# Kernel optimization log

Measured on AMD Instinct MI355X. Metric: run time of the kernel, lower is better.

## Reference

```python
import jax, jax.numpy as jnp
import numpy as np

GROUP = 128  # quantization group size along the input dimension


def dequant(q, scales, zeros):
    # q: [out, in] int4 codes stored as int32 in [0,16)
    # scales, zeros: [out, in//GROUP] per-group affine params
    out_dim, in_dim = q.shape
    g = in_dim // GROUP
    w = (q.astype(jnp.float32).reshape(out_dim, g, GROUP) - zeros[:, :, None]) * scales[:, :, None]
    return w.reshape(out_dim, in_dim)


def setup_inputs() -> dict:
    key = jax.random.key(0)
    ks = jax.random.split(key, 10)
    H, I = 4096, 11008
    B, S = 64, 1
    inp = {
        "x": jax.random.normal(ks[0], (B, S, H), dtype=jnp.float32),
        "gate_qweight": jax.random.randint(ks[1], (I, H), 0, 16, dtype=jnp.int32),
        "gate_scales": jax.random.uniform(ks[2], (I, H // GROUP), dtype=jnp.float32) * 0.02,
        "gate_zeros": jax.random.uniform(ks[3], (I, H // GROUP), dtype=jnp.float32) * 16.0,
        "up_qweight": jax.random.randint(ks[4], (I, H), 0, 16, dtype=jnp.int32),
        "up_scales": jax.random.uniform(ks[5], (I, H // GROUP), dtype=jnp.float32) * 0.02,
        "up_zeros": jax.random.uniform(ks[6], (I, H // GROUP), dtype=jnp.float32) * 16.0,
        "down_qweight": jax.random.randint(ks[7], (H, I), 0, 16, dtype=jnp.int32),
        "down_scales": jax.random.uniform(ks[8], (H, I // GROUP), dtype=jnp.float32) * 0.02,
        "down_zeros": jax.random.uniform(ks[9], (H, I // GROUP), dtype=jnp.float32) * 16.0,
    }
    return inp


def reference(x, gate_qweight, gate_scales, gate_zeros,
              up_qweight, up_scales, up_zeros,
              down_qweight, down_scales, down_zeros):
    Wg = dequant(gate_qweight, gate_scales, gate_zeros)   # [I, H]
    Wu = dequant(up_qweight, up_scales, up_zeros)         # [I, H]
    Wd = dequant(down_qweight, down_scales, down_zeros)   # [H, I]
    gate = jnp.einsum('bsh,ih->bsi', x, Wg)
    up = jnp.einsum('bsh,ih->bsi', x, Wu)
    h = jax.nn.silu(gate) * up                             # SwiGLU
    return jnp.einsum('bsi,hi->bsh', h, Wd)
```

## Files before the change

kernel.cpp:

```cpp
#include <hip/hip_runtime.h>
#include <stdint.h>

#define H_DIM 4096
#define I_DIM 11008
#define NGH   (H_DIM/128)
#define NGI   (I_DIM/128)

typedef __attribute__((ext_vector_type(8))) short short8;
typedef __attribute__((ext_vector_type(4))) float f32x4;
typedef __attribute__((ext_vector_type(4))) int   i32x4;

static __device__ __forceinline__ short f2bf(float f) {
  uint32_t u = __builtin_bit_cast(uint32_t, f);
  u = (u + 0x7FFFu + ((u >> 16) & 1u)) >> 16;
  return (short)(uint16_t)u;
}

__global__ void xcvt_kernel(const float* __restrict__ x, short* __restrict__ xb) {
  int i = blockIdx.x * 256 + threadIdx.x;
  xb[i] = f2bf(x[i]);
}

__global__ __launch_bounds__(256) void phase1_kernel(
    const short* __restrict__ xb,
    const int* __restrict__ gq, const float* __restrict__ gsc, const float* __restrict__ gze,
    const int* __restrict__ uq, const float* __restrict__ usc, const float* __restrict__ uze,
    short* __restrict__ hb)
{
  __shared__ float red[2][4][4][4][64];
  const int n0   = blockIdx.x * 16;
  const int w    = threadIdx.x >> 6;
  const int l    = threadIdx.x & 63;
  const int col  = l & 15;
  const int krow = l >> 4;
  const int i    = n0 + col;

  const int*   gqr = gq + (size_t)i * H_DIM;
  const int*   uqr = uq + (size_t)i * H_DIM;
  const float* gsr = gsc + (size_t)i * NGH;
  const float* gzr = gze + (size_t)i * NGH;
  const float* usr = usc + (size_t)i * NGH;
  const float* uzr = uze + (size_t)i * NGH;

  f32x4 accG[4], accU[4];
#pragma unroll
  for (int c = 0; c < 4; ++c)
#pragma unroll
    for (int r = 0; r < 4; ++r) { accG[c][r] = 0.f; accU[c][r] = 0.f; }

  const int g0 = w * 8;
#pragma unroll 1
  for (int g = g0; g < g0 + 8; ++g) {
    const float sg = gsr[g], zg = gzr[g] * sg;
    const float su = usr[g], zu = uzr[g] * su;
#pragma unroll
    for (int ks = 0; ks < 4; ++ks) {
      const int koff = g * 128 + ks * 32 + krow * 8;
      short8 a[4];
#pragma unroll
      for (int c = 0; c < 4; ++c)
        a[c] = *(const short8*)(xb + (size_t)(c * 16 + col) * H_DIM + koff);
      i32x4 q0 = *(const i32x4*)(gqr + koff);
      i32x4 q1 = *(const i32x4*)(gqr + koff + 4);
      i32x4 p0 = *(const i32x4*)(uqr + koff);
      i32x4 p1 = *(const i32x4*)(uqr + koff + 4);
      short8 bg, bu;
#pragma unroll
      for (int j = 0; j < 4; ++j) {
        bg[j]     = f2bf((float)q0[j] * sg - zg);
        bg[j + 4] = f2bf((float)q1[j] * sg - zg);
        bu[j]     = f2bf((float)p0[j] * su - zu);
        bu[j + 4] = f2bf((float)p1[j] * su - zu);
      }
#pragma unroll
      for (int c = 0; c < 4; ++c) {
        accG[c] = __builtin_amdgcn_mfma_f32_16x16x32_bf16(a[c], bg, accG[c], 0, 0, 0);
        accU[c] = __builtin_amdgcn_mfma_f32_16x16x32_bf16(a[c], bu, accU[c], 0, 0, 0);
      }
    }
  }

#pragma unroll
  for (int c = 0; c < 4; ++c)
#pragma unroll
    for (int r = 0; r < 4; ++r) {
      red[0][w][c][r][l] = accG[c][r];
      red[1][w][c][r][l] = accU[c][r];
    }
  __syncthreads();

  {
    const int c  = threadIdx.x >> 6;
    const int ll = threadIdx.x & 63;
#pragma unroll
    for (int r = 0; r < 4; ++r) {
      float gsum = red[0][0][c][r][ll] + red[0][1][c][r][ll]
                 + red[0][2][c][r][ll] + red[0][3][c][r][ll];
      float usum = red[1][0][c][r][ll] + red[1][1][c][r][ll]
                 + red[1][2][c][r][ll] + red[1][3][c][r][ll];
      float hv = gsum / (1.f + __expf(-gsum)) * usum;
      const int m  = c * 16 + (ll >> 4) * 4 + r;
      const int ii = n0 + (ll & 15);
      hb[(size_t)m * I_DIM + ii] = f2bf(hv);
    }
  }
}

__global__ __launch_bounds__(512) void phase2_kernel(
    const short* __restrict__ hb,
    const int* __restrict__ dq, const float* __restrict__ dsc, const float* __restrict__ dze,
    float* __restrict__ out)
{
  __shared__ float red[8][4][4][64];
  const int n0   = blockIdx.x * 16;
  const int w    = threadIdx.x >> 6;
  const int l    = threadIdx.x & 63;
  const int col  = l & 15;
  const int krow = l >> 4;
  const int n    = n0 + col;

  const int*   dqr = dq + (size_t)n * I_DIM;
  const float* dsr = dsc + (size_t)n * NGI;
  const float* dzr = dze + (size_t)n * NGI;

  f32x4 acc[4];
#pragma unroll
  for (int c = 0; c < 4; ++c)
#pragma unroll
    for (int r = 0; r < 4; ++r) acc[c][r] = 0.f;

  const int kbeg = w * (I_DIM / 8);
  int gprev = -1;
  float sv = 0.f, zv = 0.f;
#pragma unroll 1
  for (int ks = 0; ks < 43; ++ks) {
    const int k0 = kbeg + ks * 32;
    const int g  = k0 >> 7;
    if (g != gprev) { sv = dsr[g]; zv = dzr[g] * sv; gprev = g; }
    const int koff = k0 + krow * 8;
    short8 a[4];
#pragma unroll
    for (int c = 0; c < 4; ++c)
      a[c] = *(const short8*)(hb + (size_t)(c * 16 + col) * I_DIM + koff);
    i32x4 q0 = *(const i32x4*)(dqr + koff);
    i32x4 q1 = *(const i32x4*)(dqr + koff + 4);
    short8 b;
#pragma unroll
    for (int j = 0; j < 4; ++j) {
      b[j]     = f2bf((float)q0[j] * sv - zv);
      b[j + 4] = f2bf((float)q1[j] * sv - zv);
    }
#pragma unroll
    for (int c = 0; c < 4; ++c)
      acc[c] = __builtin_amdgcn_mfma_f32_16x16x32_bf16(a[c], b, acc[c], 0, 0, 0);
  }

#pragma unroll
  for (int c = 0; c < 4; ++c)
#pragma unroll
    for (int r = 0; r < 4; ++r)
      red[w][c][r][l] = acc[c][r];
  __syncthreads();

  if (threadIdx.x < 256) {
    const int c  = threadIdx.x >> 6;
    const int ll = threadIdx.x & 63;
#pragma unroll
    for (int r = 0; r < 4; ++r) {
      float s = 0.f;
#pragma unroll
      for (int ww = 0; ww < 8; ++ww) s += red[ww][c][r][ll];
      const int m  = c * 16 + (ll >> 4) * 4 + r;
      const int nn = n0 + (ll & 15);
      out[(size_t)m * H_DIM + nn] = s;
    }
  }
}

extern "C" void kernel_launch(void* const* d_in, const int* in_sizes, int n_in,
                              void* d_out, int out_size, void* d_ws, size_t ws_size,
                              hipStream_t stream) {
  const float* x  = (const float*)d_in[0];
  const int*   gq = (const int*)d_in[1];
  const float* gs = (const float*)d_in[2];
  const float* gz = (const float*)d_in[3];
  const int*   uq = (const int*)d_in[4];
  const float* us = (const float*)d_in[5];
  const float* uz = (const float*)d_in[6];
  const int*   dq = (const int*)d_in[7];
  const float* ds = (const float*)d_in[8];
  const float* dz = (const float*)d_in[9];
  float* out = (float*)d_out;

  short* xb = (short*)d_ws;
  short* hb = (short*)((char*)d_ws + (size_t)64 * H_DIM * 2);

  xcvt_kernel<<<(64 * H_DIM) / 256, 256, 0, stream>>>(x, xb);
  phase1_kernel<<<I_DIM / 16, 256, 0, stream>>>(xb, gq, gs, gz, uq, us, uz, hb);
  phase2_kernel<<<H_DIM / 16, 512, 0, stream>>>(hb, dq, ds, dz, out);
}
```

Before: 208.9 us.

## Split-K down projection, 8-wave gate/up blocks, weight prefetch, vectorized convert

Phase 2 now runs a four-way split over the intermediate dimension, launching four times as many blocks, and adds a reduce kernel that sums the partial outputs. Phase 1 moves to 512-thread blocks with eight waves splitting K and reduces gate and up through shared memory in two passes. Both phases software-prefetch the next quantized weight chunk into registers, and the x conversion is vectorized four-wide using the HIP bf16 intrinsic. The goal is more parallelism to saturate HBM on the weight stream. The cost is extra partial-buffer traffic and one more launch.

```diff
diff --git a/kernel.cpp b/kernel.cpp
--- a/kernel.cpp
+++ b/kernel.cpp
@@ -1,4 +1,5 @@
 #include <hip/hip_runtime.h>
+#include <hip/hip_bf16.h>
 #include <stdint.h>
 
 #define H_DIM 4096
@@ -7,109 +8,29 @@
 #define NGI   (I_DIM/128)
 
 typedef __attribute__((ext_vector_type(8))) short short8;
+typedef __attribute__((ext_vector_type(4))) short s16x4;
 typedef __attribute__((ext_vector_type(4))) float f32x4;
 typedef __attribute__((ext_vector_type(4))) int   i32x4;
 
 static __device__ __forceinline__ short f2bf(float f) {
-  uint32_t u = __builtin_bit_cast(uint32_t, f);
-  u = (u + 0x7FFFu + ((u >> 16) & 1u)) >> 16;
-  return (short)(uint16_t)u;
+  union { __hip_bfloat16 b; short s; } u;
+  u.b = __float2bfloat16(f);
+  return u.s;
 }
 
 __global__ void xcvt_kernel(const float* __restrict__ x, short* __restrict__ xb) {
-  int i = blockIdx.x * 256 + threadIdx.x;
-  xb[i] = f2bf(x[i]);
-}
-
-__global__ __launch_bounds__(256) void phase1_kernel(
+  int i = (blockIdx.x * 256 + threadIdx.x) * 4;
+  f32x4 v = *(const f32x4*)(x + i);
+  s16x4 o;
+  o[0] = f2bf(v[0]); o[1] = f2bf(v[1]); o[2] = f2bf(v[2]); o[3] = f2bf(v[3]);
+  *(s16x4*)(xb + i) = o;
+}
+
+__global__ __launch_bounds__(512, 4) void phase1_kernel(
     const short* __restrict__ xb,
     const int* __restrict__ gq, const float* __restrict__ gsc, const float* __restrict__ gze,
     const int* __restrict__ uq, const float* __restrict__ usc, const float* __restrict__ uze,
     short* __restrict__ hb)
-{
-  __shared__ float red[2][4][4][4][64];
-  const int n0   = blockIdx.x * 16;
-  const int w    = threadIdx.x >> 6;
-  const int l    = threadIdx.x & 63;
-  const int col  = l & 15;
-  const int krow = l >> 4;
-  const int i    = n0 + col;
-
-  const int*   gqr = gq + (size_t)i * H_DIM;
-  const int*   uqr = uq + (size_t)i * H_DIM;
-  const float* gsr = gsc + (size_t)i * NGH;
-  const float* gzr = gze + (size_t)i * NGH;
-  const float* usr = usc + (size_t)i * NGH;
-  const float* uzr = uze + (size_t)i * NGH;
-
-  f32x4 accG[4], accU[4];
-#pragma unroll
-  for (int c = 0; c < 4; ++c)
-#pragma unroll
-    for (int r = 0; r < 4; ++r) { accG[c][r] = 0.f; accU[c][r] = 0.f; }
-
-  const int g0 = w * 8;
-#pragma unroll 1
-  for (int g = g0; g < g0 + 8; ++g) {
-    const float sg = gsr[g], zg = gzr[g] * sg;
-    const float su = usr[g], zu = uzr[g] * su;
-#pragma unroll
-    for (int ks = 0; ks < 4; ++ks) {
-      const int koff = g * 128 + ks * 32 + krow * 8;
-      short8 a[4];
-#pragma unroll
-      for (int c = 0; c < 4; ++c)
-        a[c] = *(const short8*)(xb + (size_t)(c * 16 + col) * H_DIM + koff);
-      i32x4 q0 = *(const i32x4*)(gqr + koff);
-      i32x4 q1 = *(const i32x4*)(gqr + koff + 4);
-      i32x4 p0 = *(const i32x4*)(uqr + koff);
-      i32x4 p1 = *(const i32x4*)(uqr + koff + 4);
-      short8 bg, bu;
-#pragma unroll
-      for (int j = 0; j < 4; ++j) {
-        bg[j]     = f2bf((float)q0[j] * sg - zg);
-        bg[j + 4] = f2bf((float)q1[j] * sg - zg);
-        bu[j]     = f2bf((float)p0[j] * su - zu);
-        bu[j + 4] = f2bf((float)p1[j] * su - zu);
-      }
-#pragma unroll
-      for (int c = 0; c < 4; ++c) {
-        accG[c] = __builtin_amdgcn_mfma_f32_16x16x32_bf16(a[c], bg, accG[c], 0, 0, 0);
-        accU[c] = __builtin_amdgcn_mfma_f32_16x16x32_bf16(a[c], bu, accU[c], 0, 0, 0);
-      }
-    }
-  }
-
-#pragma unroll
-  for (int c = 0; c < 4; ++c)
-#pragma unroll
-    for (int r = 0; r < 4; ++r) {
-      red[0][w][c][r][l] = accG[c][r];
-      red[1][w][c][r][l] = accU[c][r];
-    }
-  __syncthreads();
-
-  {
-    const int c  = threadIdx.x >> 6;
-    const int ll = threadIdx.x & 63;
-#pragma unroll
-    for (int r = 0; r < 4; ++r) {
-      float gsum = red[0][0][c][r][ll] + red[0][1][c][r][ll]
-                 + red[0][2][c][r][ll] + red[0][3][c][r][ll];
-      float usum = red[1][0][c][r][ll] + red[1][1][c][r][ll]
-                 + red[1][2][c][r][ll] + red[1][3][c][r][ll];
-      float hv = gsum / (1.f + __expf(-gsum)) * usum;
-      const int m  = c * 16 + (ll >> 4) * 4 + r;
-      const int ii = n0 + (ll & 15);
-      hb[(size_t)m * I_DIM + ii] = f2bf(hv);
-    }
-  }
-}
-
-__global__ __launch_bounds__(512) void phase2_kernel(
-    const short* __restrict__ hb,
-    const int* __restrict__ dq, const float* __restrict__ dsc, const float* __restrict__ dze,
-    float* __restrict__ out)
 {
   __shared__ float red[8][4][4][64];
   const int n0   = blockIdx.x * 16;
@@ -117,6 +38,120 @@
   const int l    = threadIdx.x & 63;
   const int col  = l & 15;
   const int krow = l >> 4;
+  const int i    = n0 + col;
+
+  const int*   gqr = gq + (size_t)i * H_DIM;
+  const int*   uqr = uq + (size_t)i * H_DIM;
+  const float* gsr = gsc + (size_t)i * NGH;
+  const float* gzr = gze + (size_t)i * NGH;
+  const float* usr = usc + (size_t)i * NGH;
+  const float* uzr = uze + (size_t)i * NGH;
+
+  f32x4 accG[4], accU[4];
+#pragma unroll
+  for (int c = 0; c < 4; ++c)
+#pragma unroll
+    for (int r = 0; r < 4; ++r) { accG[c][r] = 0.f; accU[c][r] = 0.f; }
+
+  const int kw = w * 512;
+
+  int pk = kw + krow * 8;
+  i32x4 nq0 = *(const i32x4*)(gqr + pk);
+  i32x4 nq1 = *(const i32x4*)(gqr + pk + 4);
+  i32x4 np0 = *(const i32x4*)(uqr + pk);
+  i32x4 np1 = *(const i32x4*)(uqr + pk + 4);
+
+#pragma unroll 1
+  for (int g = 0; g < 4; ++g) {
+    const int gg = w * 4 + g;
+    const float sg = gsr[gg], zg = gzr[gg] * sg;
+    const float su = usr[gg], zu = uzr[gg] * su;
+#pragma unroll
+    for (int ks = 0; ks < 4; ++ks) {
+      i32x4 q0 = nq0, q1 = nq1, p0 = np0, p1 = np1;
+      const int klocal = g * 128 + ks * 32;
+      {
+        const int nk = kw + ((klocal + 32) & 511) + krow * 8;
+        nq0 = *(const i32x4*)(gqr + nk);
+        nq1 = *(const i32x4*)(gqr + nk + 4);
+        np0 = *(const i32x4*)(uqr + nk);
+        np1 = *(const i32x4*)(uqr + nk + 4);
+      }
+      const int koff = kw + klocal + krow * 8;
+      short8 a[4];
+#pragma unroll
+      for (int c = 0; c < 4; ++c)
+        a[c] = *(const short8*)(xb + (size_t)(c * 16 + col) * H_DIM + koff);
+      short8 bg, bu;
+#pragma unroll
+      for (int j = 0; j < 4; ++j) {
+        bg[j]     = f2bf((float)q0[j] * sg - zg);
+        bg[j + 4] = f2bf((float)q1[j] * sg - zg);
+        bu[j]     = f2bf((float)p0[j] * su - zu);
+        bu[j + 4] = f2bf((float)p1[j] * su - zu);
+      }
+#pragma unroll
+      for (int c = 0; c < 4; ++c) {
+        accG[c] = __builtin_amdgcn_mfma_f32_16x16x32_bf16(a[c], bg, accG[c], 0, 0, 0);
+        accU[c] = __builtin_amdgcn_mfma_f32_16x16x32_bf16(a[c], bu, accU[c], 0, 0, 0);
+      }
+    }
+  }
+
+  const int c2 = threadIdx.x >> 7;
+  const int rh = (threadIdx.x >> 6) & 1;
+  const int ll = threadIdx.x & 63;
+
+#pragma unroll
+  for (int c = 0; c < 4; ++c)
+#pragma unroll
+    for (int r = 0; r < 4; ++r)
+      red[w][c][r][l] = accG[c][r];
+  __syncthreads();
+  float gsum[2];
+#pragma unroll
+  for (int rr = 0; rr < 2; ++rr) {
+    const int r = rh * 2 + rr;
+    float s = 0.f;
+#pragma unroll
+    for (int ww = 0; ww < 8; ++ww) s += red[ww][c2][r][ll];
+    gsum[rr] = s;
+  }
+  __syncthreads();
+
+#pragma unroll
+  for (int c = 0; c < 4; ++c)
+#pragma unroll
+    for (int r = 0; r < 4; ++r)
+      red[w][c][r][l] = accU[c][r];
+  __syncthreads();
+#pragma unroll
+  for (int rr = 0; rr < 2; ++rr) {
+    const int r = rh * 2 + rr;
+    float us = 0.f;
+#pragma unroll
+    for (int ww = 0; ww < 8; ++ww) us += red[ww][c2][r][ll];
+    const float gv = gsum[rr];
+    const float hv = gv / (1.f + __expf(-gv)) * us;
+    const int m  = c2 * 16 + (ll >> 4) * 4 + r;
+    const int ii = n0 + (ll & 15);
+    hb[(size_t)m * I_DIM + ii] = f2bf(hv);
+  }
+}
+
+__global__ __launch_bounds__(512, 4) void phase2_kernel(
+    const short* __restrict__ hb,
+    const int* __restrict__ dq, const float* __restrict__ dsc, const float* __restrict__ dze,
+    float* __restrict__ part)
+{
+  __shared__ float red[8][4][4][64];
+  const int tile  = blockIdx.x & 255;
+  const int split = blockIdx.x >> 8;
+  const int n0   = tile * 16;
+  const int w    = threadIdx.x >> 6;
+  const int l    = threadIdx.x & 63;
+  const int col  = l & 15;
+  const int krow = l >> 4;
   const int n    = n0 + col;
 
   const int*   dqr = dq + (size_t)n * I_DIM;
@@ -129,21 +164,33 @@
 #pragma unroll
     for (int r = 0; r < 4; ++r) acc[c][r] = 0.f;
 
-  const int kbeg = w * (I_DIM / 8);
+  const int cnt    = (w < 6) ? 11 : 10;
+  const int sstart = (w < 6) ? w * 11 : 66 + (w - 6) * 10;
+  const int kbase  = split * 2752 + sstart * 32;
+
   int gprev = -1;
   float sv = 0.f, zv = 0.f;
+
+  int pk = kbase + krow * 8;
+  i32x4 nq0 = *(const i32x4*)(dqr + pk);
+  i32x4 nq1 = *(const i32x4*)(dqr + pk + 4);
+
 #pragma unroll 1
-  for (int ks = 0; ks < 43; ++ks) {
-    const int k0 = kbeg + ks * 32;
+  for (int s = 0; s < cnt; ++s) {
+    i32x4 q0 = nq0, q1 = nq1;
+    {
+      const int ns = (s + 1 < cnt) ? (s + 1) : 0;
+      const int nk = kbase + ns * 32 + krow * 8;
+      nq0 = *(const i32x4*)(dqr + nk);
+      nq1 = *(const i32x4*)(dqr + nk + 4);
+    }
+    const int k0 = kbase + s * 32;
     const int g  = k0 >> 7;
     if (g != gprev) { sv = dsr[g]; zv = dzr[g] * sv; gprev = g; }
-    const int koff = k0 + krow * 8;
     short8 a[4];
 #pragma unroll
     for (int c = 0; c < 4; ++c)
-      a[c] = *(const short8*)(hb + (size_t)(c * 16 + col) * I_DIM + koff);
-    i32x4 q0 = *(const i32x4*)(dqr + koff);
-    i32x4 q1 = *(const i32x4*)(dqr + koff + 4);
+      a[c] = *(const short8*)(hb + (size_t)(c * 16 + col) * I_DIM + k0 + krow * 8);
     short8 b;
 #pragma unroll
     for (int j = 0; j < 4; ++j) {
@@ -162,19 +209,33 @@
       red[w][c][r][l] = acc[c][r];
   __syncthreads();
 
-  if (threadIdx.x < 256) {
-    const int c  = threadIdx.x >> 6;
+  {
+    const int c2 = threadIdx.x >> 7;
+    const int rh = (threadIdx.x >> 6) & 1;
     const int ll = threadIdx.x & 63;
-#pragma unroll
-    for (int r = 0; r < 4; ++r) {
+    float* po = part + (size_t)split * (64 * H_DIM);
+#pragma unroll
+    for (int rr = 0; rr < 2; ++rr) {
+      const int r = rh * 2 + rr;
       float s = 0.f;
 #pragma unroll
-      for (int ww = 0; ww < 8; ++ww) s += red[ww][c][r][ll];
-      const int m  = c * 16 + (ll >> 4) * 4 + r;
+      for (int ww = 0; ww < 8; ++ww) s += red[ww][c2][r][ll];
+      const int m  = c2 * 16 + (ll >> 4) * 4 + r;
       const int nn = n0 + (ll & 15);
-      out[(size_t)m * H_DIM + nn] = s;
-    }
-  }
+      po[(size_t)m * H_DIM + nn] = s;
+    }
+  }
+}
+
+__global__ void reduce4_kernel(const float* __restrict__ part, float* __restrict__ out) {
+  const int idx = (blockIdx.x * 256 + threadIdx.x) * 4;
+  const int S = 64 * H_DIM;
+  f32x4 s0 = *(const f32x4*)(part + idx);
+  f32x4 s1 = *(const f32x4*)(part + S + idx);
+  f32x4 s2 = *(const f32x4*)(part + 2 * S + idx);
+  f32x4 s3 = *(const f32x4*)(part + 3 * S + idx);
+  f32x4 r = (s0 + s1) + (s2 + s3);
+  *(f32x4*)(out + idx) = r;
 }
 
 extern "C" void kernel_launch(void* const* d_in, const int* in_sizes, int n_in,
@@ -194,8 +255,10 @@
 
   short* xb = (short*)d_ws;
   short* hb = (short*)((char*)d_ws + (size_t)64 * H_DIM * 2);
-
-  xcvt_kernel<<<(64 * H_DIM) / 256, 256, 0, stream>>>(x, xb);
-  phase1_kernel<<<I_DIM / 16, 256, 0, stream>>>(xb, gq, gs, gz, uq, us, uz, hb);
-  phase2_kernel<<<H_DIM / 16, 512, 0, stream>>>(hb, dq, ds, dz, out);
-}
+  float* part = (float*)((char*)d_ws + (size_t)64 * H_DIM * 2 + (size_t)64 * I_DIM * 2);
+
+  xcvt_kernel<<<(64 * H_DIM) / 1024, 256, 0, stream>>>(x, xb);
+  phase1_kernel<<<I_DIM / 16, 512, 0, stream>>>(xb, gq, gs, gz, uq, us, uz, hb);
+  phase2_kernel<<<(H_DIM / 16) * 4, 512, 0, stream>>>(hb, dq, ds, dz, part);
+  reduce4_kernel<<<(64 * H_DIM) / 1024, 256, 0, stream>>>(part, out);
+}
```

Measured after the change: 207.7 us. About the same (-0.6%).
